# Optimization experiments

Measured on AMD Instinct MI355X. Metric: run time of the kernel, lower is better.

## Reference

```python
import jax, jax.numpy as jnp
import numpy as np

NUM_GRAPHS = 16
NODES_PER = 1024
D = 128
H = 2
KPOS = 20
E = 262144


def _ln(x, g, b):
    mu = jnp.mean(x, axis=-1, keepdims=True)
    var = jnp.mean((x - mu) ** 2, axis=-1, keepdims=True)
    return (x - mu) * jax.lax.rsqrt(var + 1e-5) * g + b


def setup_inputs() -> dict:
    key = jax.random.key(0)
    ks = jax.random.split(key, 12)
    N = NUM_GRAPHS * NODES_PER
    s = 0.02
    return {
        "x": jax.random.normal(ks[0], (N, D), jnp.float32),
        "pos_enc": jax.random.normal(ks[1], (N, KPOS), jnp.float32),
        "pe_w": jax.random.normal(ks[2], (D, KPOS), jnp.float32) * s,
        "pe_b": jnp.zeros((D,), jnp.float32),
        "in_w": jax.random.normal(ks[3], (3 * D, D), jnp.float32) * s,
        "in_b": jnp.zeros((3 * D,), jnp.float32),
        "out_w": jax.random.normal(ks[4], (D, D), jnp.float32) * s,
        "out_b": jnp.zeros((D,), jnp.float32),
        "ln1_g": jnp.ones((D,), jnp.float32),
        "ln1_b": jnp.zeros((D,), jnp.float32),
        "ln2_g": jnp.ones((D,), jnp.float32),
        "ln2_b": jnp.zeros((D,), jnp.float32),
        "ff1_w": jax.random.normal(ks[5], (4 * D, D), jnp.float32) * s,
        "ff1_b": jnp.zeros((4 * D,), jnp.float32),
        "ff2_w": jax.random.normal(ks[6], (D, 4 * D), jnp.float32) * s,
        "ff2_b": jnp.zeros((D,), jnp.float32),
        "edge_index": jax.random.randint(ks[7], (2, E), 0, N, dtype=jnp.int32),
        "batch": jnp.repeat(jnp.arange(NUM_GRAPHS, dtype=jnp.int32), NODES_PER),
    }


def reference(x, pos_enc, pe_w, pe_b, in_w, in_b, out_w, out_b,
              ln1_g, ln1_b, ln2_g, ln2_b, ff1_w, ff1_b, ff2_w, ff2_b,
              edge_index, batch):
    # pos_enc Linear + add, then per-graph transformer (graphs equal-sized -> batched)
    h = x + pos_enc @ pe_w.T + pe_b  # (N, D)
    h = h.reshape(NUM_GRAPHS, NODES_PER, D)  # (B, S, D)

    hd = D // H
    qkv = h @ in_w.T + in_b  # (B, S, 3D)
    q, k, v = jnp.split(qkv, 3, axis=-1)

    def heads(t):
        return t.reshape(NUM_GRAPHS, NODES_PER, H, hd).transpose(0, 2, 1, 3)

    q, k, v = heads(q), heads(k), heads(v)  # (B, H, S, hd)
    scores = jnp.einsum('bhqd,bhkd->bhqk', q, k) / jnp.float32(np.sqrt(hd))
    attn = jax.nn.softmax(scores, axis=-1)
    ctx = jnp.einsum('bhqk,bhkd->bhqd', attn, v)
    ctx = ctx.transpose(0, 2, 1, 3).reshape(NUM_GRAPHS, NODES_PER, D)
    sa = ctx @ out_w.T + out_b

    # post-norm (PyTorch TransformerEncoderLayer default, eval mode: no dropout)
    h = _ln(h + sa, ln1_g, ln1_b)
    ff = jax.nn.relu(h @ ff1_w.T + ff1_b) @ ff2_w.T + ff2_b
    h = _ln(h + ff, ln2_g, ln2_b)
    return h.reshape(-1, D)
```

## Files before the change

kernel.cpp:

```cpp
#include <hip/hip_runtime.h>

typedef unsigned short u16;

#define NGRAPH 16
#define SEQ    1024
#define DIM    128
#define NHEAD  2
#define HDIM   64
#define KPOS   20
#define NTOT   (NGRAPH*SEQ)
#define QKVD   (3*DIM)

__device__ __forceinline__ float bf2f(u16 u) {
    return __uint_as_float(((unsigned int)u) << 16);
}
__device__ __forceinline__ u16 f2bf(float f) {
    unsigned int u = __float_as_uint(f);
    u += 0x7fffu + ((u >> 16) & 1u);
    return (u16)(u >> 16);
}

template<int CTRL>
__device__ __forceinline__ float dpp_ror(float x) {
    return __int_as_float(__builtin_amdgcn_update_dpp(
        __float_as_int(x), __float_as_int(x), CTRL, 0xF, 0xF, true));
}
__device__ __forceinline__ float row16_max(float x) {
    x = fmaxf(x, dpp_ror<0x121>(x));
    x = fmaxf(x, dpp_ror<0x122>(x));
    x = fmaxf(x, dpp_ror<0x124>(x));
    x = fmaxf(x, dpp_ror<0x128>(x));
    return x;
}
__device__ __forceinline__ float row16_sum(float x) {
    x += dpp_ror<0x121>(x);
    x += dpp_ror<0x122>(x);
    x += dpp_ror<0x124>(x);
    x += dpp_ror<0x128>(x);
    return x;
}

__device__ __forceinline__ float ld1(const void* p, int fbf, size_t i) {
    return fbf ? bf2f(((const u16*)p)[i]) : ((const float*)p)[i];
}
__device__ __forceinline__ float4 ldw8(const void* W, int fbf, size_t i) {
    if (fbf) return *(const float4*)((const u16*)W + i);
    const float* q = (const float*)W + i;
    float4 a = *(const float4*)q, b = *(const float4*)(q + 4);
    float4 r;
    u16* d = (u16*)&r;
    d[0]=f2bf(a.x); d[1]=f2bf(a.y); d[2]=f2bf(a.z); d[3]=f2bf(a.w);
    d[4]=f2bf(b.x); d[5]=f2bf(b.y); d[6]=f2bf(b.z); d[7]=f2bf(b.w);
    return r;
}

typedef __attribute__((ext_vector_type(8))) short bf16x8;
typedef __attribute__((ext_vector_type(4))) float f32x4;

__device__ __forceinline__ void gload16(const u16* g, u16* l) {
    __builtin_amdgcn_global_load_lds(
        (const __attribute__((address_space(1))) unsigned int*)(g),
        (__attribute__((address_space(3))) unsigned int*)(l), 16, 0, 0);
}
#define VMCNT0() asm volatile("s_waitcnt vmcnt(0)" ::: "memory")

__device__ __forceinline__ int detect_bf16(const u16* x) {
    int ok = 1;
    for (int i = 0; i < 256; i += 2) {
        unsigned e = (x[i] >> 7) & 0xFF;
        if (e < 60u || e > 180u) ok = 0;
    }
    return ok;
}
__global__ void detect_kernel(const u16* __restrict__ x, int* __restrict__ flag) {
    if (threadIdx.x == 0 && blockIdx.x == 0) *flag = detect_bf16(x);
}

__global__ __launch_bounds__(256)
void wconv_kernel(const void* __restrict__ in_w, const void* __restrict__ out_w,
                  const void* __restrict__ ff1_w, const void* __restrict__ ff2_w,
                  const u16* __restrict__ x,
                  u16* __restrict__ wbf, int* __restrict__ flag) {
    __shared__ int fsh;
    if (threadIdx.x == 0) {
        int ok = detect_bf16(x);
        fsh = ok;
        if (blockIdx.x == 0) *flag = ok;
    }
    __syncthreads();
    int fbf = fsh;
    int i8 = (blockIdx.x * 256 + threadIdx.x) * 8;
    const void* src; int off;
    if      (i8 <  49152) { src = in_w;  off = i8; }
    else if (i8 <  65536) { src = out_w; off = i8 - 49152; }
    else if (i8 < 131072) { src = ff1_w; off = i8 - 65536; }
    else                  { src = ff2_w; off = i8 - 131072; }
    *(float4*)&wbf[i8] = ldw8(src, fbf, off);
}

__global__ __launch_bounds__(256)
void pe_kernel(const void* __restrict__ x, const void* __restrict__ pos,
               const void* __restrict__ pe_w, const void* __restrict__ pe_b,
               u16* __restrict__ h0, const int* __restrict__ flag) {
    int fbf = *flag;
    __shared__ float wsh[DIM][KPOS + 1];
    int t = threadIdx.x;
    for (int i = t; i < DIM * KPOS; i += 256)
        wsh[i / KPOS][i % KPOS] = ld1(pe_w, fbf, i);
    __syncthreads();
    int row = blockIdx.x * 2 + (t >> 7), d = t & 127;
    float acc = 0.f;
#pragma unroll
    for (int k = 0; k < KPOS; ++k)
        acc += ld1(pos, fbf, (size_t)row * KPOS + k) * wsh[d][k];
    int rs = fbf ? 128 : 256;
    h0[(size_t)row * rs + d] =
        f2bf(ld1(x, fbf, (size_t)row * DIM + d) + acc + ld1(pe_b, fbf, d));
}

__global__ __launch_bounds__(256)
void qkvpe_kernel(const void* __restrict__ x, const void* __restrict__ pos,
                  const void* __restrict__ pe_w, const void* __restrict__ pe_b,
                  const u16* __restrict__ W, const void* __restrict__ bias,
                  u16* __restrict__ h0, u16* __restrict__ qkv,
                  u16* __restrict__ vt, const int* __restrict__ flag) {
    int fbf = *flag;
    int rs  = fbf ? 128 : 256;
    __shared__ __align__(16) u16 Ash[64][128];
    __shared__ __align__(16) u16 Wsh[2][128][128];
    __shared__ float wsh[DIM][KPOS + 1];
    __shared__ float possh[64][KPOS + 1];
    int t = threadIdx.x;
    int w = t >> 6, lane = t & 63, l16 = lane & 15, quad = lane >> 4;
    int n0 = blockIdx.x * 64;
    int xr = (l16 & 7) << 3;

#pragma unroll
    for (int i = 0; i < 8; ++i) {
        int r = w * 4 + i * 16 + (lane >> 4);
        int s = (lane & 15) ^ (r & 7);
        gload16(&W[(size_t)r * 128 + s * 8], &Wsh[0][w * 4 + i * 16][0]);
    }
    for (int i = t; i < DIM * KPOS; i += 256)
        wsh[i / KPOS][i % KPOS] = ld1(pe_w, fbf, i);
    for (int i = t; i < 64 * KPOS; i += 256)
        possh[i / KPOS][i % KPOS] =
            ld1(pos, fbf, (size_t)(n0 + i / KPOS) * KPOS + i % KPOS);
    asm volatile("s_waitcnt lgkmcnt(0)" ::: "memory");
    __builtin_amdgcn_s_barrier();

#pragma unroll
    for (int u = 0; u < 4; ++u) {
        int gu = t + u * 256;
        int r = gu >> 4, g = gu & 15;
        float4 hv;
        u16* hp = (u16*)&hv;
#pragma unroll
        for (int j = 0; j < 8; ++j) {
            int d = g * 8 + j;
            float a = ld1(x, fbf, (size_t)(n0 + r) * DIM + d) + ld1(pe_b, fbf, d);
#pragma unroll
            for (int k = 0; k < KPOS; ++k) a += possh[r][k] * wsh[d][k];
            hp[j] = f2bf(a);
        }
        *(float4*)&Ash[r][(g ^ (r & 7)) * 8] = hv;
        *(float4*)&h0[(size_t)(n0 + r) * rs + g * 8] = hv;
    }
    asm volatile("s_waitcnt lgkmcnt(0)" ::: "memory");
    __builtin_amdgcn_s_barrier();

#pragma unroll
    for (int m = 0; m < 3; ++m) {
        int m0 = m * 128;
        if (m < 2) {
#pragma unroll
            for (int i = 0; i < 8; ++i) {
                int r = w * 4 + i * 16 + (lane >> 4);
                int s = (lane & 15) ^ (r & 7);
                gload16(&W[(size_t)(m0 + 128 + r) * 128 + s * 8],
                        &Wsh[(m + 1) & 1][w * 4 + i * 16][0]);
            }
            asm volatile("s_waitcnt vmcnt(8)" ::: "memory");
        } else {
            asm volatile("s_waitcnt vmcnt(0)" ::: "memory");
        }
        __builtin_amdgcn_s_barrier();
        f32x4 acc[8] = {};
        __builtin_amdgcn_s_setprio(1);
#pragma unroll
        for (int kk = 0; kk < 4; ++kk) {
            bf16x8 af = *(const bf16x8*)&Ash[w * 16 + l16][(kk * 32 + quad * 8) ^ xr];
#pragma unroll
            for (int s = 0; s < 8; ++s) {
                bf16x8 bf = *(const bf16x8*)&Wsh[m & 1][s * 16 + l16][(kk * 32 + quad * 8) ^ xr];
                acc[s] = __builtin_amdgcn_mfma_f32_16x16x32_bf16(af, bf, acc[s], 0, 0, 0);
            }
        }
        __builtin_amdgcn_s_setprio(0);
        float bb[8];
#pragma unroll
        for (int s = 0; s < 8; ++s) bb[s] = ld1(bias, fbf, m0 + s * 16 + l16);
#pragma unroll
        for (int r = 0; r < 4; ++r) {
            int lr = w * 16 + quad * 4 + r;
            if (m == 2) {
                int n = n0 + lr;
                int bg = n >> 10, nl = n & 1023;
#pragma unroll
                for (int s = 0; s < 8; ++s)
                    vt[((size_t)(bg * 128) + s * 16 + l16) * SEQ + nl] =
                        f2bf(acc[s][r] + bb[s]);
            } else {
#pragma unroll
                for (int s = 0; s < 8; ++s)
                    qkv[(size_t)(n0 + lr) * QKVD + m0 + s * 16 + l16] =
                        f2bf(acc[s][r] + bb[s]);
            }
        }
        if (m < 2) __builtin_amdgcn_s_barrier();
    }
}

__global__ __launch_bounds__(256)
void ffn_kernel(const u16* __restrict__ h1, const u16* __restrict__ W1,
                const u16* __restrict__ W2, const void* __restrict__ b1,
                const void* __restrict__ b2,
                const void* __restrict__ lng, const void* __restrict__ lnb,
                void* __restrict__ outp, const int* __restrict__ flag) {
    int fbf = *flag;
    int rs  = fbf ? 128 : 256;
    __shared__ __align__(16) u16 Ash[64][128];
    __shared__ __align__(16) u16 Wsh[2][128][128];
    __shared__ __align__(16) u16 F1sh[4][64][128];
    int t = threadIdx.x;
    int w = t >> 6, lane = t & 63, l16 = lane & 15, quad = lane >> 4;
    int n0 = blockIdx.x * 64;
    int xr = (l16 & 7) << 3;

#pragma unroll
    for (int i = 0; i < 4; ++i) {
        int r = w * 4 + i * 16 + (lane >> 4);
        int s = (lane & 15) ^ (r & 7);
        gload16(&h1[(size_t)(n0 + r) * rs + s * 8], &Ash[w * 4 + i * 16][0]);
    }
#pragma unroll
    for (int i = 0; i < 8; ++i) {
        int r = w * 4 + i * 16 + (lane >> 4);
        int s = (lane & 15) ^ (r & 7);
        gload16(&W1[(size_t)r * 128 + s * 8], &Wsh[0][w * 4 + i * 16][0]);
    }

#pragma unroll
    for (int m = 0; m < 4; ++m) {
#pragma unroll
        for (int i = 0; i < 8; ++i) {
            int r = w * 4 + i * 16 + (lane >> 4);
            int s = (lane & 15) ^ (r & 7);
            if (m < 3)
                gload16(&W1[(size_t)((m + 1) * 128 + r) * 128 + s * 8],
                        &Wsh[(m + 1) & 1][w * 4 + i * 16][0]);
            else
                gload16(&W2[(size_t)r * 512 + s * 8],
                        &Wsh[0][w * 4 + i * 16][0]);
        }
        asm volatile("s_waitcnt vmcnt(8)" ::: "memory");
        __builtin_amdgcn_s_barrier();
        f32x4 acc[8] = {};
        __builtin_amdgcn_s_setprio(1);
#pragma unroll
        for (int kk = 0; kk < 4; ++kk) {
            bf16x8 af = *(const bf16x8*)&Ash[w * 16 + l16][(kk * 32 + quad * 8) ^ xr];
#pragma unroll
            for (int s = 0; s < 8; ++s) {
                bf16x8 bf = *(const bf16x8*)&Wsh[m & 1][s * 16 + l16][(kk * 32 + quad * 8) ^ xr];
                acc[s] = __builtin_amdgcn_mfma_f32_16x16x32_bf16(af, bf, acc[s], 0, 0, 0);
            }
        }
        __builtin_amdgcn_s_setprio(0);
        float bb[8];
#pragma unroll
        for (int s = 0; s < 8; ++s) bb[s] = ld1(b1, fbf, m * 128 + s * 16 + l16);
#pragma unroll
        for (int r = 0; r < 4; ++r) {
            int lr = w * 16 + quad * 4 + r;
#pragma unroll
            for (int s = 0; s < 8; ++s) {
                int g = s * 2 + (l16 >> 3);
                F1sh[m][lr][((g ^ (lr & 7)) << 3) + (l16 & 7)] =
                    f2bf(fmaxf(acc[s][r] + bb[s], 0.f));
            }
        }
        asm volatile("s_waitcnt lgkmcnt(0)" ::: "memory");
        __builtin_amdgcn_s_barrier();
    }

    f32x4 acc2[8] = {};
#pragma unroll
    for (int c = 0; c < 4; ++c) {
        if (c < 3) {
#pragma unroll
            for (int i = 0; i < 8; ++i) {
                int r = w * 4 + i * 16 + (lane >> 4);
                int s = (lane & 15) ^ (r & 7);
                gload16(&W2[(size_t)r * 512 + (c + 1) * 128 + s * 8],
                        &Wsh[(c + 1) & 1][w * 4 + i * 16][0]);
            }
            asm volatile("s_waitcnt vmcnt(8)" ::: "memory");
        } else {
            asm volatile("s_waitcnt vmcnt(0)" ::: "memory");
        }
        __builtin_amdgcn_s_barrier();
        __builtin_amdgcn_s_setprio(1);
#pragma unroll
        for (int kk = 0; kk < 4; ++kk) {
            bf16x8 af = *(const bf16x8*)&F1sh[c][w * 16 + l16][(kk * 32 + quad * 8) ^ xr];
#pragma unroll
            for (int s = 0; s < 8; ++s) {
                bf16x8 bf = *(const bf16x8*)&Wsh[c & 1][s * 16 + l16][(kk * 32 + quad * 8) ^ xr];
                acc2[s] = __builtin_amdgcn_mfma_f32_16x16x32_bf16(af, bf, acc2[s], 0, 0, 0);
            }
        }
        __builtin_amdgcn_s_setprio(0);
        if (c < 3) __builtin_amdgcn_s_barrier();
    }

    float bb[8], gg[8], be[8];
#pragma unroll
    for (int s = 0; s < 8; ++s) {
        bb[s] = ld1(b2, fbf, s * 16 + l16);
        gg[s] = ld1(lng, fbf, s * 16 + l16);
        be[s] = ld1(lnb, fbf, s * 16 + l16);
    }
#pragma unroll
    for (int r = 0; r < 4; ++r) {
        int lr = w * 16 + quad * 4 + r;
        size_t rg = (size_t)(n0 + lr);
        float v[8];
#pragma unroll
        for (int s = 0; s < 8; ++s) {
            int g = s * 2 + (l16 >> 3);
            float resid = bf2f(Ash[lr][((g ^ (lr & 7)) << 3) + (l16 & 7)]);
            v[s] = acc2[s][r] + bb[s] + resid;
        }
        float sm = 0.f, sq = 0.f;
#pragma unroll
        for (int s = 0; s < 8; ++s) { sm += v[s]; sq += v[s] * v[s]; }
        sm = row16_sum(sm);
        sq = row16_sum(sq);
        float mu  = sm * (1.f / DIM);
        float var = fmaxf(sq * (1.f / DIM) - mu * mu, 0.f);
        float rsq = rsqrtf(var + 1e-5f);
        if (fbf) {
            u16* o = (u16*)outp;
#pragma unroll
            for (int s = 0; s < 8; ++s)
                o[rg * 128 + s * 16 + l16] =
                    f2bf((v[s] - mu) * rsq * gg[s] + be[s]);
        } else {
            float* o = (float*)outp;
#pragma unroll
            for (int s = 0; s < 8; ++s)
                o[rg * 128 + s * 16 + l16] =
                    (v[s] - mu) * rsq * gg[s] + be[s];
        }
    }
}

template<int EPI, int NK>
__global__ __launch_bounds__(256)
void mgemm2_kernel(const u16* __restrict__ A, const u16* __restrict__ W,
                   const void* __restrict__ bias, const u16* __restrict__ resid,
                   const void* __restrict__ lng, const void* __restrict__ lnb,
                   void* __restrict__ outp, u16* __restrict__ vt,
                   int Mtot, int AstrIn,
                   int arow0, int orow0, const int* __restrict__ flag) {
    const int K  = NK * 128;
    const int NB = (NK > 1) ? 2 : 1;
    int fbf  = *flag;
    int rs   = fbf ? 128 : 256;
    int Astr = (AstrIn < 0) ? rs : AstrIn;
    __shared__ __align__(16) u16 Ash[NB][64][128];
    __shared__ __align__(16) u16 Wsh[NB][128][128];
    int t = threadIdx.x;
    int w = t >> 6, lane = t & 63, l16 = lane & 15, quad = lane >> 4;
    int n0 = blockIdx.x * 64;
    int m0 = blockIdx.y * 128;
    int xr = (l16 & 7) << 3;
    f32x4 acc[8] = {};

    auto stage = [&](int c, int b) {
        int kc = c * 128;
#pragma unroll
        for (int i = 0; i < 4; ++i) {
            int r = w * 4 + i * 16 + (lane >> 4);
            int s = (lane & 15) ^ (r & 7);
            gload16(&A[(size_t)(arow0 + n0 + r) * Astr + kc + s * 8],
                    &Ash[b][w * 4 + i * 16][0]);
        }
#pragma unroll
        for (int i = 0; i < 8; ++i) {
            int r = w * 4 + i * 16 + (lane >> 4);
            int s = (lane & 15) ^ (r & 7);
            gload16(&W[(size_t)(m0 + r) * K + kc + s * 8],
                    &Wsh[b][w * 4 + i * 16][0]);
        }
    };

    stage(0, 0);
#pragma unroll 1
    for (int c = 0; c < NK; ++c) {
        VMCNT0();
        __syncthreads();
        if (c + 1 < NK) stage(c + 1, (c + 1) & (NB - 1));
        int b = c & (NB - 1);
        __builtin_amdgcn_s_setprio(1);
#pragma unroll
        for (int kk = 0; kk < 4; ++kk) {
            bf16x8 af = *(const bf16x8*)&Ash[b][w * 16 + l16][(kk * 32 + quad * 8) ^ xr];
#pragma unroll
            for (int s = 0; s < 8; ++s) {
                bf16x8 bf = *(const bf16x8*)&Wsh[b][s * 16 + l16][(kk * 32 + quad * 8) ^ xr];
                acc[s] = __builtin_amdgcn_mfma_f32_16x16x32_bf16(af, bf, acc[s], 0, 0, 0);
            }
        }
        __builtin_amdgcn_s_setprio(0);
    }
    float bb[8];
#pragma unroll
    for (int s = 0; s < 8; ++s) bb[s] = ld1(bias, fbf, m0 + s * 16 + l16);
    float gg[8], be[8];
    if (EPI >= 2) {
#pragma unroll
        for (int s = 0; s < 8; ++s) {
            gg[s] = ld1(lng, fbf, s * 16 + l16);
            be[s] = ld1(lnb, fbf, s * 16 + l16);
        }
    }
#pragma unroll
    for (int r = 0; r < 4; ++r) {
        int lr = w * 16 + quad * 4 + r;
        float v[8];
#pragma unroll
        for (int s = 0; s < 8; ++s) {
            v[s] = acc[s][r] + bb[s];
            if (EPI == 1) v[s] = fmaxf(v[s], 0.f);
        }
        if (EPI <= 1) {
            u16* o = (u16*)outp;
#pragma unroll
            for (int s = 0; s < 8; ++s)
                o[(size_t)(n0 + lr) * Mtot + m0 + s * 16 + l16] = f2bf(v[s]);
        } else {
            size_t rg = (size_t)(orow0 + n0 + lr);
#pragma unroll
            for (int s = 0; s < 8; ++s)
                v[s] += bf2f(resid[rg * rs + s * 16 + l16]);
            float sm = 0.f, sq = 0.f;
#pragma unroll
            for (int s = 0; s < 8; ++s) { sm += v[s]; sq += v[s] * v[s]; }
            sm = row16_sum(sm);
            sq = row16_sum(sq);
            float mu  = sm * (1.f / DIM);
            float var = fmaxf(sq * (1.f / DIM) - mu * mu, 0.f);
            float rsq = rsqrtf(var + 1e-5f);
            if (EPI == 2) {
                u16* o = (u16*)outp;
#pragma unroll
                for (int s = 0; s < 8; ++s)
                    o[rg * rs + s * 16 + l16] =
                        f2bf((v[s] - mu) * rsq * gg[s] + be[s]);
            } else {
                if (fbf) {
                    u16* o = (u16*)outp;
#pragma unroll
                    for (int s = 0; s < 8; ++s)
                        o[rg * 128 + s * 16 + l16] =
                            f2bf((v[s] - mu) * rsq * gg[s] + be[s]);
                } else {
                    float* o = (float*)outp;
#pragma unroll
                    for (int s = 0; s < 8; ++s)
                        o[rg * 128 + s * 16 + l16] =
                            (v[s] - mu) * rsq * gg[s] + be[s];
                }
            }
        }
    }
}

__global__ __launch_bounds__(256)
void attn2_kernel(const u16* __restrict__ qkv, const u16* __restrict__ vtp,
                  u16* __restrict__ ctx) {
    __shared__ __align__(16) u16 Qsh[64][72];
    __shared__ __align__(16) u16 Ksh[2][64][64];
    __shared__ __align__(16) u16 Vsh[2][64][64];
    __shared__ u16 Psh[64][72];
    int t    = threadIdx.x;
    int w    = t >> 6;
    int lane = t & 63;
    int l16  = lane & 15;
    int quad = lane >> 4;
    int xr   = (l16 & 7) << 3;
    int L = blockIdx.x;
    int ngh = gridDim.x >> 4;
    int qt, gh;
    if (ngh >= 8) {
        int g8 = L & 7; int rest = L >> 3;
        qt = rest & 15; gh = (rest >> 4) * 8 + g8;
    } else {
        qt = L & 15; gh = L >> 4;
    }
    int b = gh >> 1, h = gh & 1;

#pragma unroll
    for (int i = 0; i < 2; ++i) {
        int idx = t + i * 256;
        int r = idx >> 3, d8 = (idx & 7) * 8;
        size_t n = (size_t)b * SEQ + qt * 64 + r;
        float4 qv = *(const float4*)&qkv[n * QKVD + h * HDIM + d8];
        u16* qp = (u16*)&qv;
#pragma unroll
        for (int j = 0; j < 8; ++j) qp[j] = f2bf(bf2f(qp[j]) * 0.125f);
        *(float4*)&Qsh[r][d8] = qv;
    }

    const u16* kbase = qkv + (size_t)b * SEQ * QKVD + DIM + h * HDIM;
    const u16* vbase = vtp + (size_t)((b * 2 + h) * 64) * SEQ;

    auto stageKV = [&](int kt, int bf) {
#pragma unroll
        for (int i = 0; i < 2; ++i) {
            int r = w * 8 + i * 32 + (lane >> 3);
            int s = (lane & 7) ^ (r & 7);
            gload16(&kbase[(size_t)(kt * 64 + r) * QKVD + s * 8],
                    &Ksh[bf][w * 8 + i * 32][0]);
        }
#pragma unroll
        for (int i = 0; i < 2; ++i) {
            int r = w * 8 + i * 32 + (lane >> 3);
            int s = (lane & 7) ^ (r & 7);
            gload16(&vbase[(size_t)r * SEQ + kt * 64 + s * 8],
                    &Vsh[bf][w * 8 + i * 32][0]);
        }
    };

    stageKV(0, 0);
    VMCNT0();
    __syncthreads();
    bf16x8 qa0 = *(const bf16x8*)&Qsh[w * 16 + l16][quad * 8];
    bf16x8 qa1 = *(const bf16x8*)&Qsh[w * 16 + l16][32 + quad * 8];

    f32x4 o[4] = {};
    float mrow[4] = {-1e30f, -1e30f, -1e30f, -1e30f};
    float lrow[4] = {};

#pragma unroll 1
    for (int kt = 0; kt < SEQ / 64; ++kt) {
        int cur = kt & 1;
        if (kt + 1 < SEQ / 64) stageKV(kt + 1, cur ^ 1);

        float sc[4][4];
        __builtin_amdgcn_s_setprio(1);
#pragma unroll
        for (int c = 0; c < 4; ++c) {
            bf16x8 kb0 = *(const bf16x8*)&Ksh[cur][c * 16 + l16][(quad * 8) ^ xr];
            bf16x8 kb1 = *(const bf16x8*)&Ksh[cur][c * 16 + l16][(32 + quad * 8) ^ xr];
            f32x4 s = {};
            s = __builtin_amdgcn_mfma_f32_16x16x32_bf16(qa0, kb0, s, 0, 0, 0);
            s = __builtin_amdgcn_mfma_f32_16x16x32_bf16(qa1, kb1, s, 0, 0, 0);
#pragma unroll
            for (int r = 0; r < 4; ++r) sc[c][r] = s[r];
        }
        __builtin_amdgcn_s_setprio(0);
        float alpha[4];
#pragma unroll
        for (int r = 0; r < 4; ++r) {
            float mx = fmaxf(fmaxf(sc[0][r], sc[1][r]), fmaxf(sc[2][r], sc[3][r]));
            mx = row16_max(mx);
            float mnew = fmaxf(mrow[r], mx);
            alpha[r] = __expf(mrow[r] - mnew);
            mrow[r] = mnew;
            float sum = 0.f;
#pragma unroll
            for (int c = 0; c < 4; ++c) {
                float p = __expf(sc[c][r] - mnew);
                sc[c][r] = p;
                sum += p;
            }
            sum = row16_sum(sum);
            lrow[r] = lrow[r] * alpha[r] + sum;
        }
#pragma unroll
        for (int c = 0; c < 4; ++c)
#pragma unroll
            for (int r = 0; r < 4; ++r)
                Psh[w * 16 + quad * 4 + r][c * 16 + l16] = f2bf(sc[c][r]);
#pragma unroll
        for (int dt = 0; dt < 4; ++dt)
#pragma unroll
            for (int r = 0; r < 4; ++r) o[dt][r] *= alpha[r];
        bf16x8 pa0 = *(const bf16x8*)&Psh[w * 16 + l16][quad * 8];
        bf16x8 pa1 = *(const bf16x8*)&Psh[w * 16 + l16][32 + quad * 8];
        __builtin_amdgcn_s_setprio(1);
#pragma unroll
        for (int dt = 0; dt < 4; ++dt) {
            bf16x8 vb0 = *(const bf16x8*)&Vsh[cur][dt * 16 + l16][(quad * 8) ^ xr];
            bf16x8 vb1 = *(const bf16x8*)&Vsh[cur][dt * 16 + l16][(32 + quad * 8) ^ xr];
            o[dt] = __builtin_amdgcn_mfma_f32_16x16x32_bf16(pa0, vb0, o[dt], 0, 0, 0);
            o[dt] = __builtin_amdgcn_mfma_f32_16x16x32_bf16(pa1, vb1, o[dt], 0, 0, 0);
        }
        __builtin_amdgcn_s_setprio(0);
        if (kt + 1 < SEQ / 64) {
            VMCNT0();
            __syncthreads();
        }
    }
#pragma unroll
    for (int r = 0; r < 4; ++r) {
        float inv = 1.f / lrow[r];
        size_t n = (size_t)b * SEQ + qt * 64 + w * 16 + quad * 4 + r;
#pragma unroll
        for (int dt = 0; dt < 4; ++dt)
            ctx[n * DIM + h * HDIM + dt * 16 + l16] = f2bf(o[dt][r] * inv);
    }
}

template<int EPI, int NK>
__global__ __launch_bounds__(256)
void mgemm_kernel(const u16* __restrict__ A, const void* __restrict__ W,
                  int wbf16, const void* __restrict__ bias,
                  const u16* __restrict__ resid,
                  const void* __restrict__ lng, const void* __restrict__ lnb,
                  void* __restrict__ outp, u16* __restrict__ vt,
                  int Mtot, int AstrIn,
                  int arow0, int orow0, const int* __restrict__ flag) {
    const int K = NK * 128;
    int fbf  = *flag;
    int wfmt = wbf16 ? 1 : fbf;
    int rs   = fbf ? 128 : 256;
    int Astr = (AstrIn < 0) ? rs : AstrIn;
    __shared__ u16 Ash[64][136];
    __shared__ u16 Wsh[128][136];
    int t = threadIdx.x;
    int w = t >> 6, lane = t & 63, l16 = lane & 15, quad = lane >> 4;
    int n0 = blockIdx.x * 64;
    int m0 = blockIdx.y * 128;
    f32x4 acc[8] = {};
    float4 aR[4], wR[8];
#pragma unroll
    for (int i = 0; i < 4; ++i) {
        int idx = t + i * 256;
        int row = idx >> 4, k8 = (idx & 15) * 8;
        aR[i] = *(const float4*)&A[(size_t)(arow0 + n0 + row) * Astr + k8];
    }
#pragma unroll
    for (int i = 0; i < 8; ++i) {
        int idx = t + i * 256;
        int row = idx >> 4, k8 = (idx & 15) * 8;
        wR[i] = ldw8(W, wfmt, (size_t)(m0 + row) * K + k8);
    }
#pragma unroll 1
    for (int c = 0; c < NK; ++c) {
#pragma unroll
        for (int i = 0; i < 4; ++i) {
            int idx = t + i * 256;
            *(float4*)&Ash[idx >> 4][(idx & 15) * 8] = aR[i];
        }
#pragma unroll
        for (int i = 0; i < 8; ++i) {
            int idx = t + i * 256;
            *(float4*)&Wsh[idx >> 4][(idx & 15) * 8] = wR[i];
        }
        __syncthreads();
        if (c + 1 < NK) {
            int kc = (c + 1) * 128;
#pragma unroll
            for (int i = 0; i < 4; ++i) {
                int idx = t + i * 256;
                int row = idx >> 4, k8 = (idx & 15) * 8;
                aR[i] = *(const float4*)&A[(size_t)(arow0 + n0 + row) * Astr + kc + k8];
            }
#pragma unroll
            for (int i = 0; i < 8; ++i) {
                int idx = t + i * 256;
                int row = idx >> 4, k8 = (idx & 15) * 8;
                wR[i] = ldw8(W, wfmt, (size_t)(m0 + row) * K + kc + k8);
            }
        }
        __builtin_amdgcn_s_setprio(1);
#pragma unroll
        for (int kk = 0; kk < 4; ++kk) {
            bf16x8 af = *(const bf16x8*)&Ash[w * 16 + l16][kk * 32 + quad * 8];
#pragma unroll
            for (int s = 0; s < 8; ++s) {
                bf16x8 bf = *(const bf16x8*)&Wsh[s * 16 + l16][kk * 32 + quad * 8];
                acc[s] = __builtin_amdgcn_mfma_f32_16x16x32_bf16(af, bf, acc[s], 0, 0, 0);
            }
        }
        __builtin_amdgcn_s_setprio(0);
        if (c + 1 < NK) __syncthreads();
    }
    float bb[8];
#pragma unroll
    for (int s = 0; s < 8; ++s) bb[s] = ld1(bias, fbf, m0 + s * 16 + l16);
    float gg[8], be[8];
    if (EPI >= 2) {
#pragma unroll
        for (int s = 0; s < 8; ++s) {
            gg[s] = ld1(lng, fbf, s * 16 + l16);
            be[s] = ld1(lnb, fbf, s * 16 + l16);
        }
    }
#pragma unroll
    for (int r = 0; r < 4; ++r) {
        int lr = w * 16 + quad * 4 + r;
        float v[8];
#pragma unroll
        for (int s = 0; s < 8; ++s) {
            v[s] = acc[s][r] + bb[s];
            if (EPI == 1) v[s] = fmaxf(v[s], 0.f);
        }
        if (EPI <= 1) {
            u16* o = (u16*)outp;
#pragma unroll
            for (int s = 0; s < 8; ++s)
                o[(size_t)(n0 + lr) * Mtot + m0 + s * 16 + l16] = f2bf(v[s]);
        } else {
            size_t rg = (size_t)(orow0 + n0 + lr);
#pragma unroll
            for (int s = 0; s < 8; ++s)
                v[s] += bf2f(resid[rg * rs + s * 16 + l16]);
            float sm = 0.f, sq = 0.f;
#pragma unroll
            for (int s = 0; s < 8; ++s) { sm += v[s]; sq += v[s] * v[s]; }
            sm = row16_sum(sm);
            sq = row16_sum(sq);
            float mu  = sm * (1.f / DIM);
            float var = fmaxf(sq * (1.f / DIM) - mu * mu, 0.f);
            float rsq = rsqrtf(var + 1e-5f);
            if (EPI == 2) {
                u16* o = (u16*)outp;
#pragma unroll
                for (int s = 0; s < 8; ++s)
                    o[rg * rs + s * 16 + l16] =
                        f2bf((v[s] - mu) * rsq * gg[s] + be[s]);
            } else {
                if (fbf) {
                    u16* o = (u16*)outp;
#pragma unroll
                    for (int s = 0; s < 8; ++s)
                        o[rg * 128 + s * 16 + l16] =
                            f2bf((v[s] - mu) * rsq * gg[s] + be[s]);
                } else {
                    float* o = (float*)outp;
#pragma unroll
                    for (int s = 0; s < 8; ++s)
                        o[rg * 128 + s * 16 + l16] =
                            (v[s] - mu) * rsq * gg[s] + be[s];
                }
            }
        }
    }
}

__global__ __launch_bounds__(256)
void attn_lds_kernel(const u16* __restrict__ qkv, u16* __restrict__ ctx) {
    __shared__ u16 Qsh[64][72];
    __shared__ u16 Ksh[64][72];
    __shared__ u16 VshT[64][72];
    __shared__ u16 Psh[64][72];
    int t    = threadIdx.x;
    int w    = t >> 6;
    int lane = t & 63;
    int l16  = lane & 15;
    int quad = lane >> 4;
    int L = blockIdx.x;
    int qt = L & 15, gh = L >> 4;
    int b = gh >> 1, h = gh & 1;

#pragma unroll
    for (int i = 0; i < 2; ++i) {
        int idx = t + i * 256;
        int r = idx >> 3, d8 = (idx & 7) * 8;
        size_t n = (size_t)b * SEQ + qt * 64 + r;
        float4 qv = *(const float4*)&qkv[n * QKVD + h * HDIM + d8];
        u16* qp = (u16*)&qv;
#pragma unroll
        for (int j = 0; j < 8; ++j) qp[j] = f2bf(bf2f(qp[j]) * 0.125f);
        *(float4*)&Qsh[r][d8] = qv;
    }
    int kr = t >> 3, kd8 = (t & 7) * 8;
    int vr = t & 63, vdb = (t >> 6) * 16;
    float4 kR[2], vR[2];
    {
        size_t nk0 = (size_t)b * SEQ + kr;
        kR[0] = *(const float4*)&qkv[nk0 * QKVD + DIM + h * HDIM + kd8];
        kR[1] = *(const float4*)&qkv[(nk0 + 32) * QKVD + DIM + h * HDIM + kd8];
        size_t nv0 = (size_t)b * SEQ + vr;
        vR[0] = *(const float4*)&qkv[nv0 * QKVD + 2 * DIM + h * HDIM + vdb];
        vR[1] = *(const float4*)&qkv[nv0 * QKVD + 2 * DIM + h * HDIM + vdb + 8];
    }
    __syncthreads();
    bf16x8 qa0 = *(const bf16x8*)&Qsh[w * 16 + l16][quad * 8];
    bf16x8 qa1 = *(const bf16x8*)&Qsh[w * 16 + l16][32 + quad * 8];

    f32x4 o[4] = {};
    float mrow[4] = {-1e30f, -1e30f, -1e30f, -1e30f};
    float lrow[4] = {};

#pragma unroll 1
    for (int kt = 0; kt < SEQ / 64; ++kt) {
        *(float4*)&Ksh[kr][kd8]      = kR[0];
        *(float4*)&Ksh[kr + 32][kd8] = kR[1];
        {
            const u16* pa = (const u16*)&vR[0];
            const u16* pb = (const u16*)&vR[1];
#pragma unroll
            for (int j = 0; j < 8; ++j) VshT[vdb + j][vr] = pa[j];
#pragma unroll
            for (int j = 0; j < 8; ++j) VshT[vdb + 8 + j][vr] = pb[j];
        }
        __syncthreads();
        if (kt + 1 < SEQ / 64) {
            size_t nk0 = (size_t)b * SEQ + (kt + 1) * 64 + kr;
            kR[0] = *(const float4*)&qkv[nk0 * QKVD + DIM + h * HDIM + kd8];
            kR[1] = *(const float4*)&qkv[(nk0 + 32) * QKVD + DIM + h * HDIM + kd8];
            size_t nv0 = (size_t)b * SEQ + (kt + 1) * 64 + vr;
            vR[0] = *(const float4*)&qkv[nv0 * QKVD + 2 * DIM + h * HDIM + vdb];
            vR[1] = *(const float4*)&qkv[nv0 * QKVD + 2 * DIM + h * HDIM + vdb + 8];
        }
        float sc[4][4];
        __builtin_amdgcn_s_setprio(1);
#pragma unroll
        for (int c = 0; c < 4; ++c) {
            bf16x8 kb0 = *(const bf16x8*)&Ksh[c * 16 + l16][quad * 8];
            bf16x8 kb1 = *(const bf16x8*)&Ksh[c * 16 + l16][32 + quad * 8];
            f32x4 s = {};
            s = __builtin_amdgcn_mfma_f32_16x16x32_bf16(qa0, kb0, s, 0, 0, 0);
            s = __builtin_amdgcn_mfma_f32_16x16x32_bf16(qa1, kb1, s, 0, 0, 0);
#pragma unroll
            for (int r = 0; r < 4; ++r) sc[c][r] = s[r];
        }
        __builtin_amdgcn_s_setprio(0);
        float alpha[4];
#pragma unroll
        for (int r = 0; r < 4; ++r) {
            float mx = fmaxf(fmaxf(sc[0][r], sc[1][r]), fmaxf(sc[2][r], sc[3][r]));
            mx = row16_max(mx);
            float mnew = fmaxf(mrow[r], mx);
            alpha[r] = __expf(mrow[r] - mnew);
            mrow[r] = mnew;
            float sum = 0.f;
#pragma unroll
            for (int c = 0; c < 4; ++c) {
                float p = __expf(sc[c][r] - mnew);
                sc[c][r] = p;
                sum += p;
            }
            sum = row16_sum(sum);
            lrow[r] = lrow[r] * alpha[r] + sum;
        }
#pragma unroll
        for (int c = 0; c < 4; ++c)
#pragma unroll
            for (int r = 0; r < 4; ++r)
                Psh[w * 16 + quad * 4 + r][c * 16 + l16] = f2bf(sc[c][r]);
#pragma unroll
        for (int dt = 0; dt < 4; ++dt)
#pragma unroll
            for (int r = 0; r < 4; ++r) o[dt][r] *= alpha[r];
        bf16x8 pa0 = *(const bf16x8*)&Psh[w * 16 + l16][quad * 8];
        bf16x8 pa1 = *(const bf16x8*)&Psh[w * 16 + l16][32 + quad * 8];
        __builtin_amdgcn_s_setprio(1);
#pragma unroll
        for (int dt = 0; dt < 4; ++dt) {
            bf16x8 vb0 = *(const bf16x8*)&VshT[dt * 16 + l16][quad * 8];
            bf16x8 vb1 = *(const bf16x8*)&VshT[dt * 16 + l16][32 + quad * 8];
            o[dt] = __builtin_amdgcn_mfma_f32_16x16x32_bf16(pa0, vb0, o[dt], 0, 0, 0);
            o[dt] = __builtin_amdgcn_mfma_f32_16x16x32_bf16(pa1, vb1, o[dt], 0, 0, 0);
        }
        __builtin_amdgcn_s_setprio(0);
        __syncthreads();
    }
#pragma unroll
    for (int r = 0; r < 4; ++r) {
        float inv = 1.f / lrow[r];
        size_t n = (size_t)b * SEQ + qt * 64 + w * 16 + quad * 4 + r;
#pragma unroll
        for (int dt = 0; dt < 4; ++dt)
            ctx[n * DIM + h * HDIM + dt * 16 + l16] = f2bf(o[dt][r] * inv);
    }
}

extern "C" void kernel_launch(void* const* d_in, const int* in_sizes, int n_in,
                              void* d_out, int out_size, void* d_ws, size_t ws_size,
                              hipStream_t stream) {
    const void* x     = d_in[0];
    const void* pos   = d_in[1];
    const void* pe_w  = d_in[2];
    const void* pe_b  = d_in[3];
    const void* in_w  = d_in[4];
    const void* in_b  = d_in[5];
    const void* out_w = d_in[6];
    const void* out_b = d_in[7];
    const void* ln1_g = d_in[8];
    const void* ln1_b = d_in[9];
    const void* ln2_g = d_in[10];
    const void* ln2_b = d_in[11];
    const void* ff1_w = d_in[12];
    const void* ff1_b = d_in[13];
    const void* ff2_w = d_in[14];
    const void* ff2_b = d_in[15];

    char* wsb  = (char*)d_ws;
    int*  flag = (int*)(wsb + ((ws_size - 4) & ~(size_t)3));
    u16*  h01  = (u16*)d_out;
    const size_t MB = 1024 * 1024;

    if (ws_size >= 21 * MB) {
        u16* qkv = (u16*)wsb;
        u16* ctx = (u16*)(wsb + 12 * MB);
        u16* vt  = (u16*)(wsb + 16 * MB);
        u16* wbf = (u16*)(wsb + 20 * MB);
        u16* wb_in  = wbf;
        u16* wb_out = wbf + 49152;
        u16* wb_ff1 = wbf + 65536;
        u16* wb_ff2 = wbf + 131072;

        wconv_kernel<<<96, 256, 0, stream>>>(in_w, out_w, ff1_w, ff2_w,
                                             (const u16*)x, wbf, flag);
        qkvpe_kernel<<<NTOT / 64, 256, 0, stream>>>(
            x, pos, pe_w, pe_b, wb_in, in_b, h01, qkv, vt, flag);
        attn2_kernel<<<NGRAPH * NHEAD * 16, 256, 0, stream>>>(qkv, vt, ctx);
        mgemm2_kernel<2,1><<<dim3(NTOT / 64, 1), 256, 0, stream>>>(
            ctx, wb_out, out_b, h01, ln1_g, ln1_b, h01, nullptr,
            DIM, DIM, 0, 0, flag);
        ffn_kernel<<<NTOT / 64, 256, 0, stream>>>(
            h01, wb_ff1, wb_ff2, ff1_b, ff2_b, ln2_g, ln2_b, d_out, flag);
    } else {
        u16* qkv_g = (u16*)wsb;
        u16* ctx_g = (u16*)(wsb + 768 * 1024);
        u16* f1_g  = (u16*)wsb;
        detect_kernel<<<1, 1, 0, stream>>>((const u16*)x, flag);
        pe_kernel<<<NTOT / 2, 256, 0, stream>>>(x, pos, pe_w, pe_b, h01, flag);
        for (int g = 0; g < NGRAPH; ++g) {
            int row0 = g * SEQ;
            mgemm_kernel<0,1><<<dim3(SEQ / 64, 3), 256, 0, stream>>>(
                h01, in_w, 0, in_b, nullptr, nullptr, nullptr, qkv_g, nullptr,
                QKVD, -1, row0, 0, flag);
            attn_lds_kernel<<<NHEAD * 16, 256, 0, stream>>>(qkv_g, ctx_g);
            mgemm_kernel<2,1><<<dim3(SEQ / 64, 1), 256, 0, stream>>>(
                ctx_g, out_w, 0, out_b, h01, ln1_g, ln1_b, h01, nullptr,
                DIM, DIM, 0, row0, flag);
        }
        for (int g = 0; g < NGRAPH; ++g) {
            int row0 = g * SEQ;
            mgemm_kernel<1,1><<<dim3(SEQ / 64, 4), 256, 0, stream>>>(
                h01, ff1_w, 0, ff1_b, nullptr, nullptr, nullptr, f1_g, nullptr,
                4 * DIM, -1, row0, 0, flag);
            mgemm_kernel<3,4><<<dim3(SEQ / 64, 1), 256, 0, stream>>>(
                f1_g, ff2_w, 0, ff2_b, h01, ln2_g, ln2_b, d_out, nullptr,
                DIM, 4 * DIM, 0, row0, flag);
        }
    }
}
```

Baseline: 175.8 us.

## Fuse attention with output projection, residual and LayerNorm into one kernel

Replaces the separate attention kernel and the out-projection GEMM with one kernel. Each block processes both heads for a 64-row query tile, keeps the context in LDS, then multiplies by the output weight and applies bias, residual and LayerNorm. This removes the global context buffer round trip and one launch. In exchange, the grid drops to half as many blocks with serialized heads and a much larger LDS footprint, which reduces occupancy.

Measured after the change: 192.8 us. 9.6% more time.

```diff
diff --git a/kernel.cpp b/kernel.cpp
--- a/kernel.cpp
+++ b/kernel.cpp
@@ -222,6 +222,198 @@
 }
 
 __global__ __launch_bounds__(256)
+void attnout_kernel(const u16* __restrict__ qkv, const u16* __restrict__ vtp,
+                    const u16* __restrict__ Wout, const void* __restrict__ out_b,
+                    const void* __restrict__ lng, const void* __restrict__ lnb,
+                    u16* __restrict__ h01, const int* __restrict__ flag) {
+    int fbf = *flag;
+    int rs  = fbf ? 128 : 256;
+    __shared__ __align__(16) u16 Qsh[64][72];
+    __shared__ __align__(16) u16 Ksh[2][64][64];
+    __shared__ __align__(16) u16 Vsh[2][64][64];
+    __shared__ u16 Psh[64][72];
+    __shared__ __align__(16) u16 CtxSh[64][128];
+    __shared__ __align__(16) u16 Wsh[128][128];
+    int t    = threadIdx.x;
+    int w    = t >> 6;
+    int lane = t & 63;
+    int l16  = lane & 15;
+    int quad = lane >> 4;
+    int xr   = (l16 & 7) << 3;
+    int L = blockIdx.x;
+    int g8 = L & 7; int rest = L >> 3;
+    int qt = rest & 15; int b = (rest >> 4) * 8 + g8;
+    int n0 = b * SEQ + qt * 64;
+
+#pragma unroll
+    for (int i = 0; i < 8; ++i) {
+        int r = w * 4 + i * 16 + (lane >> 4);
+        int s = (lane & 15) ^ (r & 7);
+        gload16(&Wout[(size_t)r * 128 + s * 8], &Wsh[w * 4 + i * 16][0]);
+    }
+
+#pragma unroll 1
+    for (int h = 0; h < NHEAD; ++h) {
+#pragma unroll
+        for (int i = 0; i < 2; ++i) {
+            int idx = t + i * 256;
+            int r = idx >> 3, d8 = (idx & 7) * 8;
+            float4 qv = *(const float4*)&qkv[(size_t)(n0 + r) * QKVD + h * HDIM + d8];
+            u16* qp = (u16*)&qv;
+#pragma unroll
+            for (int j = 0; j < 8; ++j) qp[j] = f2bf(bf2f(qp[j]) * 0.125f);
+            *(float4*)&Qsh[r][d8] = qv;
+        }
+        const u16* kbase = qkv + (size_t)b * SEQ * QKVD + DIM + h * HDIM;
+        const u16* vbase = vtp + (size_t)((b * 2 + h) * 64) * SEQ;
+
+        auto stageKV = [&](int kt, int bf2) {
+#pragma unroll
+            for (int i = 0; i < 2; ++i) {
+                int r = w * 8 + i * 32 + (lane >> 3);
+                int s = (lane & 7) ^ (r & 7);
+                gload16(&kbase[(size_t)(kt * 64 + r) * QKVD + s * 8],
+                        &Ksh[bf2][w * 8 + i * 32][0]);
+            }
+#pragma unroll
+            for (int i = 0; i < 2; ++i) {
+                int r = w * 8 + i * 32 + (lane >> 3);
+                int s = (lane & 7) ^ (r & 7);
+                gload16(&vbase[(size_t)r * SEQ + kt * 64 + s * 8],
+                        &Vsh[bf2][w * 8 + i * 32][0]);
+            }
+        };
+
+        stageKV(0, 0);
+        VMCNT0();
+        __syncthreads();
+        bf16x8 qa0 = *(const bf16x8*)&Qsh[w * 16 + l16][quad * 8];
+        bf16x8 qa1 = *(const bf16x8*)&Qsh[w * 16 + l16][32 + quad * 8];
+
+        f32x4 o[4] = {};
+        float mrow[4] = {-1e30f, -1e30f, -1e30f, -1e30f};
+        float lrow[4] = {};
+
+#pragma unroll 1
+        for (int kt = 0; kt < SEQ / 64; ++kt) {
+            int cur = kt & 1;
+            if (kt + 1 < SEQ / 64) stageKV(kt + 1, cur ^ 1);
+
+            float sc[4][4];
+            __builtin_amdgcn_s_setprio(1);
+#pragma unroll
+            for (int c = 0; c < 4; ++c) {
+                bf16x8 kb0 = *(const bf16x8*)&Ksh[cur][c * 16 + l16][(quad * 8) ^ xr];
+                bf16x8 kb1 = *(const bf16x8*)&Ksh[cur][c * 16 + l16][(32 + quad * 8) ^ xr];
+                f32x4 s = {};
+                s = __builtin_amdgcn_mfma_f32_16x16x32_bf16(qa0, kb0, s, 0, 0, 0);
+                s = __builtin_amdgcn_mfma_f32_16x16x32_bf16(qa1, kb1, s, 0, 0, 0);
+#pragma unroll
+                for (int r = 0; r < 4; ++r) sc[c][r] = s[r];
+            }
+            __builtin_amdgcn_s_setprio(0);
+            float alpha[4];
+#pragma unroll
+            for (int r = 0; r < 4; ++r) {
+                float mx = fmaxf(fmaxf(sc[0][r], sc[1][r]), fmaxf(sc[2][r], sc[3][r]));
+                mx = row16_max(mx);
+                float mnew = fmaxf(mrow[r], mx);
+                alpha[r] = __expf(mrow[r] - mnew);
+                mrow[r] = mnew;
+                float sum = 0.f;
+#pragma unroll
+                for (int c = 0; c < 4; ++c) {
+                    float p = __expf(sc[c][r] - mnew);
+                    sc[c][r] = p;
+                    sum += p;
+                }
+                sum = row16_sum(sum);
+                lrow[r] = lrow[r] * alpha[r] + sum;
+            }
+#pragma unroll
+            for (int c = 0; c < 4; ++c)
+#pragma unroll
+                for (int r = 0; r < 4; ++r)
+                    Psh[w * 16 + quad * 4 + r][c * 16 + l16] = f2bf(sc[c][r]);
+#pragma unroll
+            for (int dt = 0; dt < 4; ++dt)
+#pragma unroll
+                for (int r = 0; r < 4; ++r) o[dt][r] *= alpha[r];
+            bf16x8 pa0 = *(const bf16x8*)&Psh[w * 16 + l16][quad * 8];
+            bf16x8 pa1 = *(const bf16x8*)&Psh[w * 16 + l16][32 + quad * 8];
+            __builtin_amdgcn_s_setprio(1);
+#pragma unroll
+            for (int dt = 0; dt < 4; ++dt) {
+                bf16x8 vb0 = *(const bf16x8*)&Vsh[cur][dt * 16 + l16][(quad * 8) ^ xr];
+                bf16x8 vb1 = *(const bf16x8*)&Vsh[cur][dt * 16 + l16][(32 + quad * 8) ^ xr];
+                o[dt] = __builtin_amdgcn_mfma_f32_16x16x32_bf16(pa0, vb0, o[dt], 0, 0, 0);
+                o[dt] = __builtin_amdgcn_mfma_f32_16x16x32_bf16(pa1, vb1, o[dt], 0, 0, 0);
+            }
+            __builtin_amdgcn_s_setprio(0);
+            if (kt + 1 < SEQ / 64) {
+                VMCNT0();
+                __syncthreads();
+            }
+        }
+#pragma unroll
+        for (int r = 0; r < 4; ++r) {
+            float inv = 1.f / lrow[r];
+            int lr = w * 16 + quad * 4 + r;
+#pragma unroll
+            for (int dt = 0; dt < 4; ++dt) {
+                int e = h * HDIM + dt * 16 + l16;
+                int g = e >> 3;
+                CtxSh[lr][((g ^ (lr & 7)) << 3) + (e & 7)] =
+                    f2bf(o[dt][r] * inv);
+            }
+        }
+        __syncthreads();
+    }
+
+    VMCNT0();
+    f32x4 acc[8] = {};
+    __builtin_amdgcn_s_setprio(1);
+#pragma unroll
+    for (int kk = 0; kk < 4; ++kk) {
+        bf16x8 af = *(const bf16x8*)&CtxSh[w * 16 + l16][(kk * 32 + quad * 8) ^ xr];
+#pragma unroll
+        for (int s = 0; s < 8; ++s) {
+            bf16x8 bf = *(const bf16x8*)&Wsh[s * 16 + l16][(kk * 32 + quad * 8) ^ xr];
+            acc[s] = __builtin_amdgcn_mfma_f32_16x16x32_bf16(af, bf, acc[s], 0, 0, 0);
+        }
+    }
+    __builtin_amdgcn_s_setprio(0);
+    float bb[8], gg[8], be[8];
+#pragma unroll
+    for (int s = 0; s < 8; ++s) {
+        bb[s] = ld1(out_b, fbf, s * 16 + l16);
+        gg[s] = ld1(lng, fbf, s * 16 + l16);
+        be[s] = ld1(lnb, fbf, s * 16 + l16);
+    }
+#pragma unroll
+    for (int r = 0; r < 4; ++r) {
+        int lr = w * 16 + quad * 4 + r;
+        size_t rg = (size_t)(n0 + lr);
+        float v[8];
+#pragma unroll
+        for (int s = 0; s < 8; ++s)
+            v[s] = acc[s][r] + bb[s] + bf2f(h01[rg * rs + s * 16 + l16]);
+        float sm = 0.f, sq = 0.f;
+#pragma unroll
+        for (int s = 0; s < 8; ++s) { sm += v[s]; sq += v[s] * v[s]; }
+        sm = row16_sum(sm);
+        sq = row16_sum(sq);
+        float mu  = sm * (1.f / DIM);
+        float var = fmaxf(sq * (1.f / DIM) - mu * mu, 0.f);
+        float rsq = rsqrtf(var + 1e-5f);
+#pragma unroll
+        for (int s = 0; s < 8; ++s)
+            h01[rg * rs + s * 16 + l16] =
+                f2bf((v[s] - mu) * rsq * gg[s] + be[s]);
+    }
+}
+
+__global__ __launch_bounds__(256)
 void ffn_kernel(const u16* __restrict__ h1, const u16* __restrict__ W1,
                 const u16* __restrict__ W2, const void* __restrict__ b1,
                 const void* __restrict__ b2,
@@ -363,265 +555,6 @@
                 o[rg * 128 + s * 16 + l16] =
                     (v[s] - mu) * rsq * gg[s] + be[s];
         }
-    }
-}
-
-template<int EPI, int NK>
-__global__ __launch_bounds__(256)
-void mgemm2_kernel(const u16* __restrict__ A, const u16* __restrict__ W,
-                   const void* __restrict__ bias, const u16* __restrict__ resid,
-                   const void* __restrict__ lng, const void* __restrict__ lnb,
-                   void* __restrict__ outp, u16* __restrict__ vt,
-                   int Mtot, int AstrIn,
-                   int arow0, int orow0, const int* __restrict__ flag) {
-    const int K  = NK * 128;
-    const int NB = (NK > 1) ? 2 : 1;
-    int fbf  = *flag;
-    int rs   = fbf ? 128 : 256;
-    int Astr = (AstrIn < 0) ? rs : AstrIn;
-    __shared__ __align__(16) u16 Ash[NB][64][128];
-    __shared__ __align__(16) u16 Wsh[NB][128][128];
-    int t = threadIdx.x;
-    int w = t >> 6, lane = t & 63, l16 = lane & 15, quad = lane >> 4;
-    int n0 = blockIdx.x * 64;
-    int m0 = blockIdx.y * 128;
-    int xr = (l16 & 7) << 3;
-    f32x4 acc[8] = {};
-
-    auto stage = [&](int c, int b) {
-        int kc = c * 128;
-#pragma unroll
-        for (int i = 0; i < 4; ++i) {
-            int r = w * 4 + i * 16 + (lane >> 4);
-            int s = (lane & 15) ^ (r & 7);
-            gload16(&A[(size_t)(arow0 + n0 + r) * Astr + kc + s * 8],
-                    &Ash[b][w * 4 + i * 16][0]);
-        }
-#pragma unroll
-        for (int i = 0; i < 8; ++i) {
-            int r = w * 4 + i * 16 + (lane >> 4);
-            int s = (lane & 15) ^ (r & 7);
-            gload16(&W[(size_t)(m0 + r) * K + kc + s * 8],
-                    &Wsh[b][w * 4 + i * 16][0]);
-        }
-    };
-
-    stage(0, 0);
-#pragma unroll 1
-    for (int c = 0; c < NK; ++c) {
-        VMCNT0();
-        __syncthreads();
-        if (c + 1 < NK) stage(c + 1, (c + 1) & (NB - 1));
-        int b = c & (NB - 1);
-        __builtin_amdgcn_s_setprio(1);
-#pragma unroll
-        for (int kk = 0; kk < 4; ++kk) {
-            bf16x8 af = *(const bf16x8*)&Ash[b][w * 16 + l16][(kk * 32 + quad * 8) ^ xr];
-#pragma unroll
-            for (int s = 0; s < 8; ++s) {
-                bf16x8 bf = *(const bf16x8*)&Wsh[b][s * 16 + l16][(kk * 32 + quad * 8) ^ xr];
-                acc[s] = __builtin_amdgcn_mfma_f32_16x16x32_bf16(af, bf, acc[s], 0, 0, 0);
-            }
-        }
-        __builtin_amdgcn_s_setprio(0);
-    }
-    float bb[8];
-#pragma unroll
-    for (int s = 0; s < 8; ++s) bb[s] = ld1(bias, fbf, m0 + s * 16 + l16);
-    float gg[8], be[8];
-    if (EPI >= 2) {
-#pragma unroll
-        for (int s = 0; s < 8; ++s) {
-            gg[s] = ld1(lng, fbf, s * 16 + l16);
-            be[s] = ld1(lnb, fbf, s * 16 + l16);
-        }
-    }
-#pragma unroll
-    for (int r = 0; r < 4; ++r) {
-        int lr = w * 16 + quad * 4 + r;
-        float v[8];
-#pragma unroll
-        for (int s = 0; s < 8; ++s) {
-            v[s] = acc[s][r] + bb[s];
-            if (EPI == 1) v[s] = fmaxf(v[s], 0.f);
-        }
-        if (EPI <= 1) {
-            u16* o = (u16*)outp;
-#pragma unroll
-            for (int s = 0; s < 8; ++s)
-                o[(size_t)(n0 + lr) * Mtot + m0 + s * 16 + l16] = f2bf(v[s]);
-        } else {
-            size_t rg = (size_t)(orow0 + n0 + lr);
-#pragma unroll
-            for (int s = 0; s < 8; ++s)
-                v[s] += bf2f(resid[rg * rs + s * 16 + l16]);
-            float sm = 0.f, sq = 0.f;
-#pragma unroll
-            for (int s = 0; s < 8; ++s) { sm += v[s]; sq += v[s] * v[s]; }
-            sm = row16_sum(sm);
-            sq = row16_sum(sq);
-            float mu  = sm * (1.f / DIM);
-            float var = fmaxf(sq * (1.f / DIM) - mu * mu, 0.f);
-            float rsq = rsqrtf(var + 1e-5f);
-            if (EPI == 2) {
-                u16* o = (u16*)outp;
-#pragma unroll
-                for (int s = 0; s < 8; ++s)
-                    o[rg * rs + s * 16 + l16] =
-                        f2bf((v[s] - mu) * rsq * gg[s] + be[s]);
-            } else {
-                if (fbf) {
-                    u16* o = (u16*)outp;
-#pragma unroll
-                    for (int s = 0; s < 8; ++s)
-                        o[rg * 128 + s * 16 + l16] =
-                            f2bf((v[s] - mu) * rsq * gg[s] + be[s]);
-                } else {
-                    float* o = (float*)outp;
-#pragma unroll
-                    for (int s = 0; s < 8; ++s)
-                        o[rg * 128 + s * 16 + l16] =
-                            (v[s] - mu) * rsq * gg[s] + be[s];
-                }
-            }
-        }
-    }
-}
-
-__global__ __launch_bounds__(256)
-void attn2_kernel(const u16* __restrict__ qkv, const u16* __restrict__ vtp,
-                  u16* __restrict__ ctx) {
-    __shared__ __align__(16) u16 Qsh[64][72];
-    __shared__ __align__(16) u16 Ksh[2][64][64];
-    __shared__ __align__(16) u16 Vsh[2][64][64];
-    __shared__ u16 Psh[64][72];
-    int t    = threadIdx.x;
-    int w    = t >> 6;
-    int lane = t & 63;
-    int l16  = lane & 15;
-    int quad = lane >> 4;
-    int xr   = (l16 & 7) << 3;
-    int L = blockIdx.x;
-    int ngh = gridDim.x >> 4;
-    int qt, gh;
-    if (ngh >= 8) {
-        int g8 = L & 7; int rest = L >> 3;
-        qt = rest & 15; gh = (rest >> 4) * 8 + g8;
-    } else {
-        qt = L & 15; gh = L >> 4;
-    }
-    int b = gh >> 1, h = gh & 1;
-
-#pragma unroll
-    for (int i = 0; i < 2; ++i) {
-        int idx = t + i * 256;
-        int r = idx >> 3, d8 = (idx & 7) * 8;
-        size_t n = (size_t)b * SEQ + qt * 64 + r;
-        float4 qv = *(const float4*)&qkv[n * QKVD + h * HDIM + d8];
-        u16* qp = (u16*)&qv;
-#pragma unroll
-        for (int j = 0; j < 8; ++j) qp[j] = f2bf(bf2f(qp[j]) * 0.125f);
-        *(float4*)&Qsh[r][d8] = qv;
-    }
-
-    const u16* kbase = qkv + (size_t)b * SEQ * QKVD + DIM + h * HDIM;
-    const u16* vbase = vtp + (size_t)((b * 2 + h) * 64) * SEQ;
-
-    auto stageKV = [&](int kt, int bf) {
-#pragma unroll
-        for (int i = 0; i < 2; ++i) {
-            int r = w * 8 + i * 32 + (lane >> 3);
-            int s = (lane & 7) ^ (r & 7);
-            gload16(&kbase[(size_t)(kt * 64 + r) * QKVD + s * 8],
-                    &Ksh[bf][w * 8 + i * 32][0]);
-        }
-#pragma unroll
-        for (int i = 0; i < 2; ++i) {
-            int r = w * 8 + i * 32 + (lane >> 3);
-            int s = (lane & 7) ^ (r & 7);
-            gload16(&vbase[(size_t)r * SEQ + kt * 64 + s * 8],
-                    &Vsh[bf][w * 8 + i * 32][0]);
-        }
-    };
-
-    stageKV(0, 0);
-    VMCNT0();
-    __syncthreads();
-    bf16x8 qa0 = *(const bf16x8*)&Qsh[w * 16 + l16][quad * 8];
-    bf16x8 qa1 = *(const bf16x8*)&Qsh[w * 16 + l16][32 + quad * 8];
-
-    f32x4 o[4] = {};
-    float mrow[4] = {-1e30f, -1e30f, -1e30f, -1e30f};
-    float lrow[4] = {};
-
-#pragma unroll 1
-    for (int kt = 0; kt < SEQ / 64; ++kt) {
-        int cur = kt & 1;
-        if (kt + 1 < SEQ / 64) stageKV(kt + 1, cur ^ 1);
-
-        float sc[4][4];
-        __builtin_amdgcn_s_setprio(1);
-#pragma unroll
-        for (int c = 0; c < 4; ++c) {
-            bf16x8 kb0 = *(const bf16x8*)&Ksh[cur][c * 16 + l16][(quad * 8) ^ xr];
-            bf16x8 kb1 = *(const bf16x8*)&Ksh[cur][c * 16 + l16][(32 + quad * 8) ^ xr];
-            f32x4 s = {};
-            s = __builtin_amdgcn_mfma_f32_16x16x32_bf16(qa0, kb0, s, 0, 0, 0);
-            s = __builtin_amdgcn_mfma_f32_16x16x32_bf16(qa1, kb1, s, 0, 0, 0);
-#pragma unroll
-            for (int r = 0; r < 4; ++r) sc[c][r] = s[r];
-        }
-        __builtin_amdgcn_s_setprio(0);
-        float alpha[4];
-#pragma unroll
-        for (int r = 0; r < 4; ++r) {
-            float mx = fmaxf(fmaxf(sc[0][r], sc[1][r]), fmaxf(sc[2][r], sc[3][r]));
-            mx = row16_max(mx);
-            float mnew = fmaxf(mrow[r], mx);
-            alpha[r] = __expf(mrow[r] - mnew);
-            mrow[r] = mnew;
-            float sum = 0.f;
-#pragma unroll
-            for (int c = 0; c < 4; ++c) {
-                float p = __expf(sc[c][r] - mnew);
-                sc[c][r] = p;
-                sum += p;
-            }
-            sum = row16_sum(sum);
-            lrow[r] = lrow[r] * alpha[r] + sum;
-        }
-#pragma unroll
-        for (int c = 0; c < 4; ++c)
-#pragma unroll
-            for (int r = 0; r < 4; ++r)
-                Psh[w * 16 + quad * 4 + r][c * 16 + l16] = f2bf(sc[c][r]);
-#pragma unroll
-        for (int dt = 0; dt < 4; ++dt)
-#pragma unroll
-            for (int r = 0; r < 4; ++r) o[dt][r] *= alpha[r];
-        bf16x8 pa0 = *(const bf16x8*)&Psh[w * 16 + l16][quad * 8];
-        bf16x8 pa1 = *(const bf16x8*)&Psh[w * 16 + l16][32 + quad * 8];
-        __builtin_amdgcn_s_setprio(1);
-#pragma unroll
-        for (int dt = 0; dt < 4; ++dt) {
-            bf16x8 vb0 = *(const bf16x8*)&Vsh[cur][dt * 16 + l16][(quad * 8) ^ xr];
-            bf16x8 vb1 = *(const bf16x8*)&Vsh[cur][dt * 16 + l16][(32 + quad * 8) ^ xr];
-            o[dt] = __builtin_amdgcn_mfma_f32_16x16x32_bf16(pa0, vb0, o[dt], 0, 0, 0);
-            o[dt] = __builtin_amdgcn_mfma_f32_16x16x32_bf16(pa1, vb1, o[dt], 0, 0, 0);
-        }
-        __builtin_amdgcn_s_setprio(0);
-        if (kt + 1 < SEQ / 64) {
-            VMCNT0();
-            __syncthreads();
-        }
-    }
-#pragma unroll
-    for (int r = 0; r < 4; ++r) {
-        float inv = 1.f / lrow[r];
-        size_t n = (size_t)b * SEQ + qt * 64 + w * 16 + quad * 4 + r;
-#pragma unroll
-        for (int dt = 0; dt < 4; ++dt)
-            ctx[n * DIM + h * HDIM + dt * 16 + l16] = f2bf(o[dt][r] * inv);
     }
 }
 
@@ -919,7 +852,6 @@
 
     if (ws_size >= 21 * MB) {
         u16* qkv = (u16*)wsb;
-        u16* ctx = (u16*)(wsb + 12 * MB);
         u16* vt  = (u16*)(wsb + 16 * MB);
         u16* wbf = (u16*)(wsb + 20 * MB);
         u16* wb_in  = wbf;
@@ -931,10 +863,8 @@
                                              (const u16*)x, wbf, flag);
         qkvpe_kernel<<<NTOT / 64, 256, 0, stream>>>(
             x, pos, pe_w, pe_b, wb_in, in_b, h01, qkv, vt, flag);
-        attn2_kernel<<<NGRAPH * NHEAD * 16, 256, 0, stream>>>(qkv, vt, ctx);
-        mgemm2_kernel<2,1><<<dim3(NTOT / 64, 1), 256, 0, stream>>>(
-            ctx, wb_out, out_b, h01, ln1_g, ln1_b, h01, nullptr,
-            DIM, DIM, 0, 0, flag);
+        attnout_kernel<<<NTOT / 64, 256, 0, stream>>>(
+            qkv, vt, wb_out, out_b, ln1_g, ln1_b, h01, flag);
         ffn_kernel<<<NTOT / 64, 256, 0, stream>>>(
             h01, wb_ff1, wb_ff2, ff1_b, ff2_b, ln2_g, ln2_b, d_out, flag);
     } else {
```
